# Kernel tuning notes

Measured on AMD Instinct MI355X. Metric: run time of the kernel, lower is better.

Reference implementation:

```python
import jax, jax.numpy as jnp
import numpy as np

B, H, W, C = 4, 256, 256, 256
WS = 8          # window size (both dims)
HEADS = 1
SEQ = WS * WS   # 64 tokens per window
NW = B * (H // WS) * (W // WS)  # 4096 windows
INNER = C * HEADS


def setup_inputs() -> dict:
    key = jax.random.key(0)
    k1, k2, k3, k4 = jax.random.split(key, 4)
    x = jax.random.normal(k1, (B, H, W, C), dtype=jnp.float32)
    attn = jax.random.uniform(k2, (NW, HEADS, SEQ, SEQ), dtype=jnp.float32)
    # to_v: Linear(dim, inner_dim, bias=False); stored as [in, out] for x @ Wv
    Wv = jax.random.normal(k3, (C, INNER), dtype=jnp.float32) * (C ** -0.5)
    # to_out: Linear(inner_dim, dim)
    Wo = jax.random.normal(k4, (INNER, C), dtype=jnp.float32) * (INNER ** -0.5)
    bo = jnp.zeros((C,), dtype=jnp.float32)
    return {"x": x, "attn": attn, "Wv": Wv, "Wo": Wo, "bo": bo}


def reference(x, attn, Wv, Wo, bo):
    b, h, w, c = x.shape
    nh, nw = h // WS, w // WS
    # window partition: b (h b0) (w b1) c -> (b h w) (b0 b1) c
    xw = x.reshape(b, nh, WS, nw, WS, c).transpose(0, 1, 3, 2, 4, 5)
    xw = xw.reshape(b * nh * nw, SEQ, c)
    # value projection, split heads: n s (h d) -> n h s d
    v = (xw @ Wv).reshape(-1, SEQ, HEADS, c).transpose(0, 2, 1, 3)
    # precomputed-attention weighted sum
    out = jnp.einsum('nhij,nhjd->nhid', attn, v)
    # merge heads: n h s d -> n s (h d)
    out = out.transpose(0, 2, 1, 3).reshape(-1, SEQ, HEADS * c)
    out = out @ Wo + bo
    # window un-partition: (b h w) (b0 b1) c -> b (h b0) (w b1) c
    out = out.reshape(b, nh, nw, WS, WS, c).transpose(0, 1, 3, 2, 4, 5)
    return out.reshape(b, h, w, c)
```

## Files before the change

### kernel.cpp

```cpp
#include <hip/hip_runtime.h>
#include <hip/hip_bf16.h>


typedef __bf16 bf16x8 __attribute__((ext_vector_type(8)));
typedef __bf16 bf16x4 __attribute__((ext_vector_type(4)));
typedef float  f32x16 __attribute__((ext_vector_type(16)));
typedef float  f32x4  __attribute__((ext_vector_type(4)));
typedef unsigned int uint;
typedef uint   uint4v __attribute__((ext_vector_type(4)));

#define MFMA32(a, b, c) __builtin_amdgcn_mfma_f32_32x32x16_bf16(a, b, c, 0, 0, 0)

__global__ void wfuse_kernel(const float* __restrict__ Wv,
                             const float* __restrict__ Wo,
                             __bf16* __restrict__ WT) {
  const int n = blockIdx.x;
  const int k = threadIdx.x;
  const float* wvrow = Wv + k * 256;
  float acc = 0.f;
#pragma unroll 4
  for (int j = 0; j < 256; j += 4) {
    f32x4 wv = *(const f32x4*)(wvrow + j);
    acc += wv.x * Wo[(j + 0) * 256 + n];
    acc += wv.y * Wo[(j + 1) * 256 + n];
    acc += wv.z * Wo[(j + 2) * 256 + n];
    acc += wv.w * Wo[(j + 3) * 256 + n];
  }
  WT[n * 256 + k] = (__bf16)acc;
}

static __device__ __forceinline__ uint pkbf(float lo, float hi) {
  return (uint)__builtin_bit_cast(unsigned short, (__bf16)lo) |
         ((uint)__builtin_bit_cast(unsigned short, (__bf16)hi) << 16);
}

static __device__ __forceinline__ void build_bfrags(const f32x16 acc, int lh,
                                                    bf16x8* bf) {
  uint wd0 = pkbf(acc[0],  acc[1]);
  uint wd1 = pkbf(acc[2],  acc[3]);
  uint wd2 = pkbf(acc[4],  acc[5]);
  uint wd3 = pkbf(acc[6],  acc[7]);
  uint wd4 = pkbf(acc[8],  acc[9]);
  uint wd5 = pkbf(acc[10], acc[11]);
  uint wd6 = pkbf(acc[12], acc[13]);
  uint wd7 = pkbf(acc[14], acc[15]);
  {
    uint o0 = (uint)__shfl_xor((int)wd2, 32);
    uint o1 = (uint)__shfl_xor((int)wd3, 32);
    uint o2 = (uint)__shfl_xor((int)wd0, 32);
    uint o3 = (uint)__shfl_xor((int)wd1, 32);
    uint4v uv = { lh ? o0 : wd0, lh ? o1 : wd1,
                  lh ? wd2 : o2, lh ? wd3 : o3 };
    bf[0] = __builtin_bit_cast(bf16x8, uv);
  }
  {
    uint o0 = (uint)__shfl_xor((int)wd6, 32);
    uint o1 = (uint)__shfl_xor((int)wd7, 32);
    uint o2 = (uint)__shfl_xor((int)wd4, 32);
    uint o3 = (uint)__shfl_xor((int)wd5, 32);
    uint4v uv = { lh ? o0 : wd4, lh ? o1 : wd5,
                  lh ? wd6 : o2, lh ? wd7 : o3 };
    bf[1] = __builtin_bit_cast(bf16x8, uv);
  }
}

static __device__ __forceinline__ long wbase(int w) {
  int wi = w & 31;
  int hi = (w >> 5) & 31;
  int b  = w >> 10;
  return (((long)(b * 256 + hi * 8)) * 256 + wi * 8) * 256;
}

static __device__ __forceinline__ void dma16(const float* gp, char* lp) {
  __builtin_amdgcn_global_load_lds(
      (const __attribute__((address_space(1))) uint*)gp,
      (__attribute__((address_space(3))) uint*)lp, 16, 0, 0);
}

static __device__ __forceinline__ bf16x8 ldax(const char* xs, int tok, int g) {
  const int sw = tok & 31;
  f32x4 u = *(const f32x4*)(xs + tok * 1024 + ((g ^ sw) << 4));
  f32x4 v = *(const f32x4*)(xs + tok * 1024 + (((g + 1) ^ sw) << 4));
  bf16x8 r;
  r[0] = (__bf16)u.x; r[1] = (__bf16)u.y; r[2] = (__bf16)u.z; r[3] = (__bf16)u.w;
  r[4] = (__bf16)v.x; r[5] = (__bf16)v.y; r[6] = (__bf16)v.z; r[7] = (__bf16)v.w;
  return r;
}

__global__ __launch_bounds__(512, 2)
void na_msa_kernel(const float* __restrict__ x,
                   const float* __restrict__ attn,
                   const __bf16* __restrict__ WT,
                   const float* __restrict__ bo,
                   float* __restrict__ out) {
  __shared__ char lds[147456];

  const int t    = threadIdx.x;
  const int lane = t & 63;
  const int wvi  = t >> 6;
  const int ln31 = lane & 31;
  const int lh   = lane >> 5;

  const __bf16* wtp = WT + (wvi * 32 + ln31) * 256 + 8 * lh;
  const float bv = bo[wvi * 32 + ln31];

  const int arow0 = t >> 4;
  const int ak0   = (t & 15) * 4;

  const int w0 = blockIdx.x * 16;

#define STAGE_X(W, BUFOFF) do {                                            \
    const float* xp_ = x + wbase(W);                                       \
    _Pragma("unroll")                                                      \
    for (int j = 0; j < 8; ++j) {                                          \
      int tok_ = j * 8 + wvi;                                              \
      int ch0_ = (lane ^ (tok_ & 31)) * 4;                                 \
      const float* gp_ = xp_ + (tok_ >> 3) * 65536 + (tok_ & 7) * 256 + ch0_; \
      int off_ = __builtin_amdgcn_readfirstlane((BUFOFF) + j * 8192 + wvi * 1024); \
      dma16(gp_, lds + off_);                                              \
    } } while (0)

#define AWR(BAT, R0, R1) do {                                              \
    *(bf16x4*)((BAT) + arow0 * 128 + ((ak0 * 2) ^ ((arow0 & 7) << 4))) =   \
        bf16x4{ (__bf16)(R0).x, (__bf16)(R0).y, (__bf16)(R0).z, (__bf16)(R0).w }; \
    int row1_ = 32 + arow0;                                                \
    *(bf16x4*)((BAT) + row1_ * 128 + ((ak0 * 2) ^ ((row1_ & 7) << 4))) =   \
        bf16x4{ (__bf16)(R1).x, (__bf16)(R1).y, (__bf16)(R1).z, (__bf16)(R1).w }; \
    } while (0)

  bf16x8 wb[16];
#pragma unroll
  for (int ks = 0; ks < 16; ++ks) wb[ks] = *(const bf16x8*)(wtp + ks * 16);

  {
    const float* ap = attn + (long)w0 * 4096;
    f32x4 a0 = *(const f32x4*)(ap + t * 4);
    f32x4 a1 = *(const f32x4*)(ap + (512 + t) * 4);
    AWR(lds + 131072, a0, a1);
    STAGE_X(w0, 0);
  }
  asm volatile("s_waitcnt vmcnt(0) lgkmcnt(0)" ::: "memory");
  __builtin_amdgcn_s_barrier();
  __builtin_amdgcn_sched_barrier(0);

#pragma unroll 1
  for (int i = 0; i < 16; ++i) {
    const int w = w0 + i;
    const char* xs = lds + (i & 1) * 65536;
    const char* as = lds + 131072 + (i & 1) * 8192;

    f32x4 ra0, ra1;
    if (i < 15) {
      const float* ap = attn + (long)(w + 1) * 4096;
      ra0 = *(const f32x4*)(ap + t * 4);
      ra1 = *(const f32x4*)(ap + (512 + t) * 4);
      STAGE_X(w + 1, ((i + 1) & 1) * 65536);
    }
    __builtin_amdgcn_sched_barrier(0);

    f32x16 acc0 = {}, acc1 = {};
#pragma unroll
    for (int ks = 0; ks < 16; ++ks) {
      int g = 4 * ks + 2 * lh;
      bf16x8 a0 = ldax(xs, ln31, g);
      bf16x8 a1 = ldax(xs, 32 + ln31, g);
      acc0 = MFMA32(a0, wb[ks], acc0);
      acc1 = MFMA32(a1, wb[ks], acc1);
    }

    bf16x8 bfr[4];
    build_bfrags(acc0, lh, &bfr[0]);
    build_bfrags(acc1, lh, &bfr[2]);

    f32x16 o0 = {}, o1 = {};
#pragma unroll
    for (int ks = 0; ks < 4; ++ks) {
      int kk = ks * 16 + 8 * lh;
      int ab0 = ln31 * 128 + ((kk * 2) ^ ((ln31 & 7) << 4));
      bf16x8 a0 = *(const bf16x8*)(as + ab0);
      bf16x8 a1 = *(const bf16x8*)(as + ab0 + 4096);
      o0 = MFMA32(a0, bfr[ks], o0);
      o1 = MFMA32(a1, bfr[ks], o1);
    }

    {
      float* op = out + wbase(w);
      const int ch = wvi * 32 + ln31;
#pragma unroll
      for (int r = 0; r < 16; ++r) {
        int tok = (r & 3) + 8 * (r >> 2) + 4 * lh;
        op[(tok >> 3) * 65536 + (tok & 7) * 256 + ch] = o0[r] + bv;
      }
#pragma unroll
      for (int r = 0; r < 16; ++r) {
        int tok = 32 + (r & 3) + 8 * (r >> 2) + 4 * lh;
        op[(tok >> 3) * 65536 + (tok & 7) * 256 + ch] = o1[r] + bv;
      }
    }

    if (i < 15) {
      AWR(lds + 131072 + ((i + 1) & 1) * 8192, ra0, ra1);
    }

    asm volatile("s_waitcnt vmcnt(32) lgkmcnt(0)" ::: "memory");
    __builtin_amdgcn_s_barrier();
    __builtin_amdgcn_sched_barrier(0);
  }
#undef STAGE_X
#undef AWR
}

extern "C" void kernel_launch(void* const* d_in, const int* in_sizes, int n_in,
                              void* d_out, int out_size, void* d_ws, size_t ws_size,
                              hipStream_t stream) {
  const float* x    = (const float*)d_in[0];
  const float* attn = (const float*)d_in[1];
  const float* Wv   = (const float*)d_in[2];
  const float* Wo   = (const float*)d_in[3];
  const float* bo   = (const float*)d_in[4];
  float* out = (float*)d_out;
  __bf16* WT = (__bf16*)d_ws;

  wfuse_kernel<<<256, 256, 0, stream>>>(Wv, Wo, WT);
  na_msa_kernel<<<256, 512, 0, stream>>>(x, attn, WT, bo, out);
}
```

Measured before the change: 156.1 us.

## Split x staging into channel halves to shrink LDS and double block count

The LDS buffer for each window's x tile is split into two 128-channel halves, staged and consumed in turn, replacing the full double-buffered 64 KB tiles. This cuts shared memory from about 144 KB to 80 KB per block, so the grid doubles to 512 blocks of 8 windows each, with launch bounds asking for more resident blocks. The goal is more overlap and more parallel blocks for this memory-bound kernel. In exchange each window needs an extra full barrier and vmcnt(0) wait, and the prefetch distance gets shorter.

```diff
diff --git a/kernel.cpp b/kernel.cpp
--- a/kernel.cpp
+++ b/kernel.cpp
@@ -77,23 +77,23 @@
       (__attribute__((address_space(3))) uint*)lp, 16, 0, 0);
 }
 
-static __device__ __forceinline__ bf16x8 ldax(const char* xs, int tok, int g) {
+static __device__ __forceinline__ bf16x8 ldax_h(const char* xs, int tok, int g) {
   const int sw = tok & 31;
-  f32x4 u = *(const f32x4*)(xs + tok * 1024 + ((g ^ sw) << 4));
-  f32x4 v = *(const f32x4*)(xs + tok * 1024 + (((g + 1) ^ sw) << 4));
+  f32x4 u = *(const f32x4*)(xs + tok * 512 + ((g ^ sw) << 4));
+  f32x4 v = *(const f32x4*)(xs + tok * 512 + (((g + 1) ^ sw) << 4));
   bf16x8 r;
   r[0] = (__bf16)u.x; r[1] = (__bf16)u.y; r[2] = (__bf16)u.z; r[3] = (__bf16)u.w;
   r[4] = (__bf16)v.x; r[5] = (__bf16)v.y; r[6] = (__bf16)v.z; r[7] = (__bf16)v.w;
   return r;
 }
 
-__global__ __launch_bounds__(512, 2)
+__global__ __launch_bounds__(512, 4)
 void na_msa_kernel(const float* __restrict__ x,
                    const float* __restrict__ attn,
                    const __bf16* __restrict__ WT,
                    const float* __restrict__ bo,
                    float* __restrict__ out) {
-  __shared__ char lds[147456];
+  __shared__ char lds[81920];
 
   const int t    = threadIdx.x;
   const int lane = t & 63;
@@ -107,16 +107,18 @@
   const int arow0 = t >> 4;
   const int ak0   = (t & 15) * 4;
 
-  const int w0 = blockIdx.x * 16;
-
-#define STAGE_X(W, BUFOFF) do {                                            \
+  const int w0 = blockIdx.x * 8;
+
+#define STAGE_XH(W, HALF, BUFOFF) do {                                     \
     const float* xp_ = x + wbase(W);                                       \
     _Pragma("unroll")                                                      \
-    for (int j = 0; j < 8; ++j) {                                          \
-      int tok_ = j * 8 + wvi;                                              \
-      int ch0_ = (lane ^ (tok_ & 31)) * 4;                                 \
-      const float* gp_ = xp_ + (tok_ >> 3) * 65536 + (tok_ & 7) * 256 + ch0_; \
-      int off_ = __builtin_amdgcn_readfirstlane((BUFOFF) + j * 8192 + wvi * 1024); \
+    for (int jj = 0; jj < 4; ++jj) {                                       \
+      int tp_ = jj * 8 + wvi;                                              \
+      int tok_ = tp_ * 2 + (lane >> 5);                                    \
+      int perm_ = (lane & 31) ^ (tok_ & 31);                               \
+      const float* gp_ = xp_ + (tok_ >> 3) * 65536 + (tok_ & 7) * 256 +    \
+                         (HALF) * 128 + perm_ * 4;                         \
+      int off_ = __builtin_amdgcn_readfirstlane((BUFOFF) + tp_ * 1024);    \
       dma16(gp_, lds + off_);                                              \
     } } while (0)
 
@@ -136,34 +138,48 @@
     const float* ap = attn + (long)w0 * 4096;
     f32x4 a0 = *(const f32x4*)(ap + t * 4);
     f32x4 a1 = *(const f32x4*)(ap + (512 + t) * 4);
-    AWR(lds + 131072, a0, a1);
-    STAGE_X(w0, 0);
+    STAGE_XH(w0, 0, 0);
+    AWR(lds + 65536, a0, a1);
   }
   asm volatile("s_waitcnt vmcnt(0) lgkmcnt(0)" ::: "memory");
   __builtin_amdgcn_s_barrier();
   __builtin_amdgcn_sched_barrier(0);
 
 #pragma unroll 1
-  for (int i = 0; i < 16; ++i) {
+  for (int i = 0; i < 8; ++i) {
     const int w = w0 + i;
-    const char* xs = lds + (i & 1) * 65536;
-    const char* as = lds + 131072 + (i & 1) * 8192;
+    const char* as = lds + 65536 + (i & 1) * 8192;
 
     f32x4 ra0, ra1;
-    if (i < 15) {
+    if (i < 7) {
       const float* ap = attn + (long)(w + 1) * 4096;
       ra0 = *(const f32x4*)(ap + t * 4);
       ra1 = *(const f32x4*)(ap + (512 + t) * 4);
-      STAGE_X(w + 1, ((i + 1) & 1) * 65536);
-    }
+    }
+    STAGE_XH(w, 1, 32768);
     __builtin_amdgcn_sched_barrier(0);
 
     f32x16 acc0 = {}, acc1 = {};
 #pragma unroll
-    for (int ks = 0; ks < 16; ++ks) {
+    for (int ks = 0; ks < 8; ++ks) {
       int g = 4 * ks + 2 * lh;
-      bf16x8 a0 = ldax(xs, ln31, g);
-      bf16x8 a1 = ldax(xs, 32 + ln31, g);
+      bf16x8 a0 = ldax_h(lds, ln31, g);
+      bf16x8 a1 = ldax_h(lds, 32 + ln31, g);
+      acc0 = MFMA32(a0, wb[ks], acc0);
+      acc1 = MFMA32(a1, wb[ks], acc1);
+    }
+    asm volatile("s_waitcnt vmcnt(0) lgkmcnt(0)" ::: "memory");
+    __builtin_amdgcn_s_barrier();
+    __builtin_amdgcn_sched_barrier(0);
+
+    if (i < 7) STAGE_XH(w + 1, 0, 0);
+    __builtin_amdgcn_sched_barrier(0);
+
+#pragma unroll
+    for (int ks = 8; ks < 16; ++ks) {
+      int g = 4 * (ks - 8) + 2 * lh;
+      bf16x8 a0 = ldax_h(lds + 32768, ln31, g);
+      bf16x8 a1 = ldax_h(lds + 32768, 32 + ln31, g);
       acc0 = MFMA32(a0, wb[ks], acc0);
       acc1 = MFMA32(a1, wb[ks], acc1);
     }
@@ -183,6 +199,11 @@
       o1 = MFMA32(a1, bfr[ks], o1);
     }
 
+    if (i < 7) {
+      AWR(lds + 65536 + ((i + 1) & 1) * 8192, ra0, ra1);
+    }
+    __builtin_amdgcn_sched_barrier(0);
+
     {
       float* op = out + wbase(w);
       const int ch = wvi * 32 + ln31;
@@ -198,15 +219,11 @@
       }
     }
 
-    if (i < 15) {
-      AWR(lds + 131072 + ((i + 1) & 1) * 8192, ra0, ra1);
-    }
-
     asm volatile("s_waitcnt vmcnt(32) lgkmcnt(0)" ::: "memory");
     __builtin_amdgcn_s_barrier();
     __builtin_amdgcn_sched_barrier(0);
   }
-#undef STAGE_X
+#undef STAGE_XH
 #undef AWR
 }
 
@@ -222,5 +239,5 @@
   __bf16* WT = (__bf16*)d_ws;
 
   wfuse_kernel<<<256, 256, 0, stream>>>(Wv, Wo, WT);
-  na_msa_kernel<<<256, 512, 0, stream>>>(x, attn, WT, bo, out);
-}
+  na_msa_kernel<<<512, 512, 0, stream>>>(x, attn, WT, bo, out);
+}
```

New measurement: 321.1 us. 2.06x slower.
